# Kernel optimization log

Measured on AMD Instinct MI355X. Metric: run time of the kernel, lower is better.

## Reference

```python
import jax, jax.numpy as jnp
import numpy as np

WIN = 8        # window_size
HEADS = 8      # n_heads
SHIFT = WIN // 2

# relative position index (static buffer, n_dim=2)
_coords = np.stack(np.meshgrid(np.arange(WIN), np.arange(WIN), indexing='ij'), 0).reshape(2, WIN * WIN)
_rel = _coords[:, :, None] - _coords[:, None, :] + (WIN - 1)          # [2, w*w, w*w]
REL_IDX = _rel[0] * (2 * WIN - 1) + _rel[1]                            # [w*w, w*w] int


def setup_inputs() -> dict:
    key = jax.random.key(0)
    ks = jax.random.split(key, 6)
    B, C, H, W = 4, 256, 128, 128
    x = jax.random.normal(ks[0], (B, C, H, W), dtype=jnp.float32)
    w_qkv = jax.random.normal(ks[1], (C, 3 * C), dtype=jnp.float32) * 0.02
    b_qkv = jax.random.normal(ks[2], (3 * C,), dtype=jnp.float32) * 0.02
    w_out = jax.random.normal(ks[3], (C, C), dtype=jnp.float32) * 0.02
    b_out = jax.random.normal(ks[4], (C,), dtype=jnp.float32) * 0.02
    bias_table = jax.random.normal(ks[5], ((2 * WIN - 1) ** 2, HEADS), dtype=jnp.float32) * 0.02
    return {"x": x, "w_qkv": w_qkv, "b_qkv": b_qkv, "w_out": w_out, "b_out": b_out, "bias_table": bias_table}


def reference(x, w_qkv, b_qkv, w_out, b_out, bias_table):
    B, C, H, W = x.shape
    w = WIN
    ch = C // HEADS
    xf = jnp.moveaxis(x, 1, -1)                                # [B,H,W,C]
    xf = jnp.roll(xf, (-SHIFT, -SHIFT), axis=(1, 2))           # shifted windows (cyclic)
    # H,W chosen divisible by window_size -> no circular padding needed
    qkv = xf @ w_qkv + b_qkv                                   # [B,H,W,3C]
    Hw, Ww = H // w, W // w
    # contiguous window partition -> [B, nWin, w*w, 3, heads, ch]
    qkv = qkv.reshape(B, Hw, w, Ww, w, 3 * C).transpose(0, 1, 3, 2, 4, 5)
    qkv = qkv.reshape(B, Hw * Ww, w * w, 3, HEADS, ch)
    q = jnp.moveaxis(qkv[..., 0, :, :], -2, 2)                 # [B,nWin,heads,seq,ch]
    k = jnp.moveaxis(qkv[..., 1, :, :], -2, 2)
    v = jnp.moveaxis(qkv[..., 2, :, :], -2, 2)
    bias = bias_table[REL_IDX]                                 # [seq,seq,heads]
    bias = jnp.transpose(bias, (2, 0, 1))                      # [heads,seq,seq]
    scale = 1.0 / jnp.sqrt(jnp.asarray(ch, dtype=q.dtype))
    scores = jnp.einsum('bnhsc,bnhtc->bnhst', q, k) * scale + bias
    attn = jax.nn.softmax(scores, axis=-1)
    out = jnp.einsum('bnhst,bnhtc->bnhsc', attn, v)            # [B,nWin,heads,seq,ch]
    out = jnp.moveaxis(out, 2, -2).reshape(B, Hw, Ww, w, w, C) # merge heads
    out = out.transpose(0, 1, 3, 2, 4, 5).reshape(B, H, W, C)  # un-window
    out = jnp.roll(out, (SHIFT, SHIFT), axis=(1, 2))           # undo shift
    out = out @ w_out + b_out                                  # [B,H,W,Cout]
    return jnp.moveaxis(out, -1, 1)                            # [B,Cout,H,W]
```

## Files before the change

### kernel.cpp

```cpp
#include <hip/hip_runtime.h>

typedef float  f32x4  __attribute__((ext_vector_type(4)));
typedef __bf16 bf16x8 __attribute__((ext_vector_type(8)));
typedef __bf16 bf16x2 __attribute__((ext_vector_type(2)));
typedef short  s16x8  __attribute__((ext_vector_type(8)));
typedef unsigned u32x4 __attribute__((ext_vector_type(4)));

static __device__ __forceinline__ unsigned short f2bf(float f) {
  unsigned u = __builtin_bit_cast(unsigned, f);
  u += 0x7FFFu + ((u >> 16) & 1u);
  return (unsigned short)(u >> 16);
}

static __device__ __forceinline__ unsigned pk2(float a, float b) {
  bf16x2 v = { (__bf16)a, (__bf16)b };
  return __builtin_bit_cast(unsigned, v);
}

static __device__ __forceinline__ f32x4 mfma16(s16x8 a, s16x8 b, f32x4 c) {
  return __builtin_amdgcn_mfma_f32_16x16x32_bf16(
      __builtin_bit_cast(bf16x8, a), __builtin_bit_cast(bf16x8, b), c, 0, 0, 0);
}

static __device__ __forceinline__ void gll16(const void* g, void* lds) {
  __builtin_amdgcn_global_load_lds(
      (const __attribute__((address_space(1))) unsigned int*)g,
      (__attribute__((address_space(3))) unsigned int*)lds, 16, 0, 0);
}

__global__ __launch_bounds__(256) void k_conv_x(const float* __restrict__ x,
                                                unsigned short* __restrict__ xb) {
  __shared__ __align__(16) unsigned short L[512 * 40];
  int bid = blockIdx.x;
  int cchunk = bid & 7, h2 = (bid >> 3) & 1, wy = (bid >> 4) & 15, b = bid >> 8;
  int t = threadIdx.x;
  int cpair = t >> 7, slot = t & 127, lr = slot >> 5, lp = slot & 31;
  int y = (wy * 8 + h2 * 4 + lr + 4) & 127;
  const float* row0 = x + ((size_t)b << 22) + (y << 7);
  int cbase = cchunk * 32;

  for (int it = 0; it < 8; ++it) {
    int cL0 = it * 4 + cpair * 2;
    const float* pa = row0 + ((size_t)(cbase + cL0) << 14) + lp * 4;
    f32x4 a  = *reinterpret_cast<const f32x4*>(pa);
    f32x4 c4 = *reinterpret_cast<const f32x4*>(pa + 16384);
#pragma unroll
    for (int i = 0; i < 4; ++i) {
      int xc = lp * 4 + i;
      int xp = (xc - 4) & 127;
      int wx = xp >> 3, ix = xp & 7;
      int sg = lr * 128 + ix * 16 + wx;
      unsigned pk = (unsigned)f2bf(a[i]) | ((unsigned)f2bf(c4[i]) << 16);
      *reinterpret_cast<unsigned*>(&L[sg * 40 + cL0]) = pk;
    }
  }
  __syncthreads();

  size_t M0 = ((size_t)((b * 16 + wy) * 16)) * 64 + h2 * 32;
  for (int pass = 0; pass < 8; ++pass) {
    int tk = pass * 64 + (t >> 2), p = t & 3;
    int wx = tk >> 5, lr2 = (tk >> 3) & 3, ix = tk & 7;
    int sg = lr2 * 128 + ix * 16 + wx;
    uint4 v = *reinterpret_cast<const uint4*>(&L[sg * 40 + p * 8]);
    size_t m = M0 + (size_t)wx * 64 + lr2 * 8 + ix;
    *reinterpret_cast<uint4*>(&xb[m * 256 + cbase + p * 8]) = v;
  }
}

__global__ __launch_bounds__(256) void k_conv_w(const float* __restrict__ wqkv,
                                                const float* __restrict__ wout,
                                                unsigned short* __restrict__ wqkvT,
                                                unsigned short* __restrict__ woutT) {
  int j = blockIdx.x, c = threadIdx.x;
  if (j < 768) wqkvT[j * 256 + c] = f2bf(wqkv[c * 768 + j]);
  else { int jj = j - 768; woutT[jj * 256 + c] = f2bf(wout[c * 256 + jj]); }
}

__global__ __launch_bounds__(256) void k_bias(const float* __restrict__ btab,
                                              float* __restrict__ bmat) {
  int i = blockIdx.x * 256 + threadIdx.x;
  int t = i & 63, s = (i >> 6) & 63, h = i >> 12;
  int idx = ((s >> 3) - (t >> 3) + 7) * 15 + ((s & 7) - (t & 7) + 7);
  bmat[i] = btab[idx * 8 + h];
}

__global__ __launch_bounds__(256, 4) void k_qkvattn(const unsigned short* __restrict__ xb,
                                                    const unsigned short* __restrict__ wT,
                                                    const float* __restrict__ bqkv,
                                                    const float* __restrict__ bmat,
                                                    unsigned short* __restrict__ ao) {
  __shared__ __align__(16) unsigned char smA[32768];
  int lane = threadIdx.x & 63, w = threadIdx.x >> 6;
  int bid = blockIdx.x;
  int sb = (bid & 7) * 256 + (bid >> 3);
  int win = sb >> 1, h = (sb & 1) * 4 + w;
  int g = lane >> 4, l15 = lane & 15;
  int m0 = win * 64;
  const float scale = 0.17677669529663687f;

#pragma unroll
  for (int i = 0; i < 8; ++i) {
    int inst = w * 8 + i;
    int row = inst * 2 + (lane >> 5);
    int sg = (lane & 31) ^ (row & 7);
    gll16(xb + (size_t)(m0 + row) * 256 + sg * 8, smA + inst * 1024);
  }
  __syncthreads();

  const unsigned short* Wq = wT + (size_t)(h * 32 + l15) * 256 + g * 8;
  const unsigned short* Wk = Wq + 65536;
  const unsigned short* Wv = Wk + 65536;

  f32x4 aQ[2][4], aK[2][4];
#pragma unroll
  for (int jt = 0; jt < 2; ++jt)
#pragma unroll
    for (int mt = 0; mt < 4; ++mt) {
      aQ[jt][mt] = f32x4{0.f, 0.f, 0.f, 0.f};
      aK[jt][mt] = f32x4{0.f, 0.f, 0.f, 0.f};
    }
#pragma unroll
  for (int ks = 0; ks < 8; ++ks) {
    int off = ks * 32;
    s16x8 fq[2], fk[2];
#pragma unroll
    for (int jt = 0; jt < 2; ++jt) {
      fq[jt] = *reinterpret_cast<const s16x8*>(Wq + (size_t)jt * 4096 + off);
      fk[jt] = *reinterpret_cast<const s16x8*>(Wk + (size_t)jt * 4096 + off);
    }
    s16x8 af[4];
#pragma unroll
    for (int mt = 0; mt < 4; ++mt) {
      int row = mt * 16 + l15;
      int chunk = (ks * 4 + g) ^ (row & 7);
      af[mt] = *reinterpret_cast<const s16x8*>(smA + row * 512 + chunk * 16);
    }
    __builtin_amdgcn_s_setprio(1);
#pragma unroll
    for (int jt = 0; jt < 2; ++jt)
#pragma unroll
      for (int mt = 0; mt < 4; ++mt) {
        aQ[jt][mt] = mfma16(fq[jt], af[mt], aQ[jt][mt]);
        aK[jt][mt] = mfma16(fk[jt], af[mt], aK[jt][mt]);
      }
    __builtin_amdgcn_s_setprio(0);
  }

  f32x4 bq2[2], bk2[2];
#pragma unroll
  for (int jt = 0; jt < 2; ++jt) {
    bq2[jt] = *reinterpret_cast<const f32x4*>(&bqkv[h * 32 + jt * 16 + g * 4]);
    bk2[jt] = *reinterpret_cast<const f32x4*>(&bqkv[256 + h * 32 + jt * 16 + g * 4]);
  }
  s16x8 kfr[4], qfr[4];
#pragma unroll
  for (int ti = 0; ti < 4; ++ti) {
    u32x4 uk, uq;
    uk[0] = pk2(aK[0][ti][0] + bk2[0][0], aK[0][ti][1] + bk2[0][1]);
    uk[1] = pk2(aK[0][ti][2] + bk2[0][2], aK[0][ti][3] + bk2[0][3]);
    uk[2] = pk2(aK[1][ti][0] + bk2[1][0], aK[1][ti][1] + bk2[1][1]);
    uk[3] = pk2(aK[1][ti][2] + bk2[1][2], aK[1][ti][3] + bk2[1][3]);
    kfr[ti] = __builtin_bit_cast(s16x8, uk);
    uq[0] = pk2((aQ[0][ti][0] + bq2[0][0]) * scale, (aQ[0][ti][1] + bq2[0][1]) * scale);
    uq[1] = pk2((aQ[0][ti][2] + bq2[0][2]) * scale, (aQ[0][ti][3] + bq2[0][3]) * scale);
    uq[2] = pk2((aQ[1][ti][0] + bq2[1][0]) * scale, (aQ[1][ti][1] + bq2[1][1]) * scale);
    uq[3] = pk2((aQ[1][ti][2] + bq2[1][2]) * scale, (aQ[1][ti][3] + bq2[1][3]) * scale);
    qfr[ti] = __builtin_bit_cast(s16x8, uq);
  }

  f32x4 aV[4][2];
#pragma unroll
  for (int mt = 0; mt < 4; ++mt)
#pragma unroll
    for (int ni = 0; ni < 2; ++ni) aV[mt][ni] = f32x4{0.f, 0.f, 0.f, 0.f};
#pragma unroll
  for (int ks = 0; ks < 8; ++ks) {
    int off = ks * 32;
    s16x8 fv[2];
#pragma unroll
    for (int jt = 0; jt < 2; ++jt)
      fv[jt] = *reinterpret_cast<const s16x8*>(Wv + (size_t)jt * 4096 + off);
    s16x8 af[4];
#pragma unroll
    for (int mt = 0; mt < 4; ++mt) {
      int row = mt * 16 + l15;
      int chunk = (ks * 4 + g) ^ (row & 7);
      af[mt] = *reinterpret_cast<const s16x8*>(smA + row * 512 + chunk * 16);
    }
    __builtin_amdgcn_s_setprio(1);
#pragma unroll
    for (int mt = 0; mt < 4; ++mt)
#pragma unroll
      for (int ni = 0; ni < 2; ++ni)
        aV[mt][ni] = mfma16(af[mt], fv[ni], aV[mt][ni]);
    __builtin_amdgcn_s_setprio(0);
  }

  float bv2[2];
  bv2[0] = bqkv[512 + h * 32 + l15];
  bv2[1] = bqkv[512 + h * 32 + 16 + l15];
  s16x8 vfr[2][2];
#pragma unroll
  for (int ni = 0; ni < 2; ++ni)
#pragma unroll
    for (int ks = 0; ks < 2; ++ks) {
      u32x4 uv;
      uv[0] = pk2(aV[2 * ks][ni][0] + bv2[ni], aV[2 * ks][ni][1] + bv2[ni]);
      uv[1] = pk2(aV[2 * ks][ni][2] + bv2[ni], aV[2 * ks][ni][3] + bv2[ni]);
      uv[2] = pk2(aV[2 * ks + 1][ni][0] + bv2[ni], aV[2 * ks + 1][ni][1] + bv2[ni]);
      uv[3] = pk2(aV[2 * ks + 1][ni][2] + bv2[ni], aV[2 * ks + 1][ni][3] + bv2[ni]);
      vfr[ni][ks] = __builtin_bit_cast(s16x8, uv);
    }

  const float* bm = bmat + (h << 12);
  f32x4 sbf[4][4];
#pragma unroll
  for (int ti = 0; ti < 4; ++ti)
#pragma unroll
    for (int si = 0; si < 4; ++si)
      sbf[ti][si] = *reinterpret_cast<const f32x4*>(&bm[(si * 16 + l15) * 64 + ti * 16 + g * 4]);

  f32x4 st[4][4];
  __builtin_amdgcn_s_setprio(1);
#pragma unroll
  for (int ti = 0; ti < 4; ++ti)
#pragma unroll
    for (int si = 0; si < 4; ++si)
      st[ti][si] = mfma16(kfr[ti], qfr[si], sbf[ti][si]);
  __builtin_amdgcn_s_setprio(0);

  unsigned pw[4][4][2];
#pragma unroll
  for (int si = 0; si < 4; ++si) {
    float mx = st[0][si][0];
#pragma unroll
    for (int ti = 0; ti < 4; ++ti)
#pragma unroll
      for (int r = 0; r < 4; ++r) mx = fmaxf(mx, st[ti][si][r]);
    mx = fmaxf(mx, __shfl_xor(mx, 16));
    mx = fmaxf(mx, __shfl_xor(mx, 32));
    float p[4][4];
    float sum = 0.f;
#pragma unroll
    for (int ti = 0; ti < 4; ++ti)
#pragma unroll
      for (int r = 0; r < 4; ++r) {
        p[ti][r] = __expf(st[ti][si][r] - mx);
        sum += p[ti][r];
      }
    sum += __shfl_xor(sum, 16);
    sum += __shfl_xor(sum, 32);
    float inv = 1.0f / sum;
#pragma unroll
    for (int ti = 0; ti < 4; ++ti) {
      pw[ti][si][0] = pk2(p[ti][0] * inv, p[ti][1] * inv);
      pw[ti][si][1] = pk2(p[ti][2] * inv, p[ti][3] * inv);
    }
  }

  f32x4 ot[2][4];
#pragma unroll
  for (int ni = 0; ni < 2; ++ni)
#pragma unroll
    for (int mi = 0; mi < 4; ++mi) ot[ni][mi] = f32x4{0.f, 0.f, 0.f, 0.f};
  __builtin_amdgcn_s_setprio(1);
#pragma unroll
  for (int ks = 0; ks < 2; ++ks) {
#pragma unroll
    for (int mi = 0; mi < 4; ++mi) {
      u32x4 up;
      up[0] = pw[2 * ks][mi][0];
      up[1] = pw[2 * ks][mi][1];
      up[2] = pw[2 * ks + 1][mi][0];
      up[3] = pw[2 * ks + 1][mi][1];
      s16x8 pf = __builtin_bit_cast(s16x8, up);
#pragma unroll
      for (int ni = 0; ni < 2; ++ni)
        ot[ni][mi] = mfma16(vfr[ni][ks], pf, ot[ni][mi]);
    }
  }
  __builtin_amdgcn_s_setprio(0);

#pragma unroll
  for (int ni = 0; ni < 2; ++ni)
#pragma unroll
    for (int mi = 0; mi < 4; ++mi) {
      uint2 pk;
      pk.x = pk2(ot[ni][mi][0], ot[ni][mi][1]);
      pk.y = pk2(ot[ni][mi][2], ot[ni][mi][3]);
      size_t m = (size_t)(win * 64 + mi * 16 + l15);
      *reinterpret_cast<uint2*>(&ao[m * 256 + h * 32 + ni * 16 + g * 4]) = pk;
    }
}

__global__ __launch_bounds__(256) void k_oproj(const unsigned short* __restrict__ ao,
                                               const unsigned short* __restrict__ wT,
                                               const float* __restrict__ bout,
                                               float* __restrict__ out) {
  __shared__ __align__(16) unsigned short Al[128 * 64];
  __shared__ __align__(16) unsigned short Bl[128 * 64];
  int j0 = blockIdx.x * 128, m0 = blockIdx.y * 128;
  int lane = threadIdx.x & 63, w = threadIdx.x >> 6;
  int wm = w >> 1, wn = w & 1, g = lane >> 4, l15 = lane & 15;

  f32x4 acc[4][4];
#pragma unroll
  for (int i = 0; i < 4; ++i)
#pragma unroll
    for (int j = 0; j < 4; ++j) acc[i][j] = f32x4{0.f, 0.f, 0.f, 0.f};

  for (int kt = 0; kt < 4; ++kt) {
    int k0 = kt * 64;
#pragma unroll
    for (int i = 0; i < 4; ++i) {
      int r0 = (w * 4 + i) * 8;
      int row = r0 + (lane >> 3);
      int sg = (lane & 7) ^ (row & 7);
      gll16(ao + (size_t)(m0 + row) * 256 + k0 + sg * 8, &Al[r0 * 64]);
      gll16(wT + (size_t)(j0 + row) * 256 + k0 + sg * 8, &Bl[r0 * 64]);
    }
    __syncthreads();
#pragma unroll
    for (int ks = 0; ks < 2; ++ks) {
      s16x8 af[4], bf[4];
#pragma unroll
      for (int mi = 0; mi < 4; ++mi) {
        int row = wm * 64 + mi * 16 + l15;
        int chunk = (ks * 4 + g) ^ (row & 7);
        af[mi] = *reinterpret_cast<const s16x8*>(&Al[row * 64 + chunk * 8]);
      }
#pragma unroll
      for (int ni = 0; ni < 4; ++ni) {
        int row = wn * 64 + ni * 16 + l15;
        int chunk = (ks * 4 + g) ^ (row & 7);
        bf[ni] = *reinterpret_cast<const s16x8*>(&Bl[row * 64 + chunk * 8]);
      }
#pragma unroll
      for (int mi = 0; mi < 4; ++mi)
#pragma unroll
        for (int ni = 0; ni < 4; ++ni)
          acc[mi][ni] = mfma16(af[mi], bf[ni], acc[mi][ni]);
    }
    __syncthreads();
  }

#pragma unroll
  for (int ni = 0; ni < 4; ++ni) {
    int j = j0 + wn * 64 + ni * 16 + l15;
    float bj = bout[j];
#pragma unroll
    for (int mi = 0; mi < 4; ++mi) {
      int mb = m0 + wm * 64 + mi * 16 + g * 4;
      int win = mb >> 6, seq0 = mb & 63;
      int b = win >> 8, wy = (win >> 4) & 15, wx = win & 15;
      int iy = seq0 >> 3, ix0 = seq0 & 7;
      int y = (wy * 8 + iy + 4) & 127;
      int x0 = (wx * 8 + ix0 + 4) & 127;
      f32x4 v = acc[mi][ni];
      v.x += bj; v.y += bj; v.z += bj; v.w += bj;
      *reinterpret_cast<f32x4*>(&out[(((size_t)b * 256 + j) << 14) + (y << 7) + x0]) = v;
    }
  }
}

extern "C" void kernel_launch(void* const* d_in, const int* in_sizes, int n_in,
                              void* d_out, int out_size, void* d_ws, size_t ws_size,
                              hipStream_t stream) {
  const float* x    = (const float*)d_in[0];
  const float* wqkv = (const float*)d_in[1];
  const float* bqkv = (const float*)d_in[2];
  const float* wout = (const float*)d_in[3];
  const float* bout = (const float*)d_in[4];
  const float* btab = (const float*)d_in[5];
  float* out = (float*)d_out;
  char* ws = (char*)d_ws;

  unsigned short* XB = (unsigned short*)(ws);
  unsigned short* AO = (unsigned short*)(ws + 33554432);
  unsigned short* WQ = (unsigned short*)(ws + 67108864);
  unsigned short* WO = (unsigned short*)(ws + 67502080);
  float*          BM = (float*)(ws + 67633152);
  if (ws_size < 67764224ull) return;

  k_conv_x<<<1024, 256, 0, stream>>>(x, XB);
  k_conv_w<<<1024, 256, 0, stream>>>(wqkv, wout, WQ, WO);
  k_bias<<<128, 256, 0, stream>>>(btab, BM);
  k_qkvattn<<<2048, 256, 0, stream>>>(XB, WQ, bqkv, BM, AO);
  k_oproj<<<dim3(2, 512), 256, 0, stream>>>(AO, WO, bout, out);
}
```

Before: 137.6 us.

## Split window attention into two key halves with online softmax rescaling

The 64-key score computation is split into two 32-key halves. Each half computes scores, does a partial softmax and immediately feeds its P·V MFMA, and the second half rescales the running output and sum in the flash-attention style. Normalization by the final sum moves to the output store. This lowers register pressure, since only a half score tile and not the full 4x4 tile plus bias is live at once, and it lets MFMA overlap with softmax ALU work. The cost is extra exp and rescale operations and more shuffles.

Measured after the change: 135.0 us. Within noise of the previous version (-1.9%).

```diff
diff --git a/kernel.cpp b/kernel.cpp
--- a/kernel.cpp
+++ b/kernel.cpp
@@ -213,81 +213,98 @@
     }
 
   const float* bm = bmat + (h << 12);
-  f32x4 sbf[4][4];
-#pragma unroll
-  for (int ti = 0; ti < 4; ++ti)
-#pragma unroll
-    for (int si = 0; si < 4; ++si)
-      sbf[ti][si] = *reinterpret_cast<const f32x4*>(&bm[(si * 16 + l15) * 64 + ti * 16 + g * 4]);
-
-  f32x4 st[4][4];
-  __builtin_amdgcn_s_setprio(1);
-#pragma unroll
-  for (int ti = 0; ti < 4; ++ti)
-#pragma unroll
-    for (int si = 0; si < 4; ++si)
-      st[ti][si] = mfma16(kfr[ti], qfr[si], sbf[ti][si]);
-  __builtin_amdgcn_s_setprio(0);
-
-  unsigned pw[4][4][2];
-#pragma unroll
-  for (int si = 0; si < 4; ++si) {
-    float mx = st[0][si][0];
-#pragma unroll
-    for (int ti = 0; ti < 4; ++ti)
-#pragma unroll
-      for (int r = 0; r < 4; ++r) mx = fmaxf(mx, st[ti][si][r]);
-    mx = fmaxf(mx, __shfl_xor(mx, 16));
-    mx = fmaxf(mx, __shfl_xor(mx, 32));
-    float p[4][4];
-    float sum = 0.f;
-#pragma unroll
-    for (int ti = 0; ti < 4; ++ti)
-#pragma unroll
-      for (int r = 0; r < 4; ++r) {
-        p[ti][r] = __expf(st[ti][si][r] - mx);
-        sum += p[ti][r];
-      }
-    sum += __shfl_xor(sum, 16);
-    sum += __shfl_xor(sum, 32);
-    float inv = 1.0f / sum;
-#pragma unroll
-    for (int ti = 0; ti < 4; ++ti) {
-      pw[ti][si][0] = pk2(p[ti][0] * inv, p[ti][1] * inv);
-      pw[ti][si][1] = pk2(p[ti][2] * inv, p[ti][3] * inv);
-    }
-  }
-
   f32x4 ot[2][4];
 #pragma unroll
   for (int ni = 0; ni < 2; ++ni)
 #pragma unroll
     for (int mi = 0; mi < 4; ++mi) ot[ni][mi] = f32x4{0.f, 0.f, 0.f, 0.f};
-  __builtin_amdgcn_s_setprio(1);
-#pragma unroll
-  for (int ks = 0; ks < 2; ++ks) {
+
+  float m01[4], s01[4], inv[4];
+
+  {
+    f32x4 sth[2][4];
+    __builtin_amdgcn_s_setprio(1);
+#pragma unroll
+    for (int th = 0; th < 2; ++th)
+#pragma unroll
+      for (int si = 0; si < 4; ++si)
+        sth[th][si] = mfma16(kfr[th], qfr[si], f32x4{0.f, 0.f, 0.f, 0.f});
+    __builtin_amdgcn_s_setprio(0);
+#pragma unroll
+    for (int si = 0; si < 4; ++si) {
+      int srow = (si * 16 + l15) * 64;
+      f32x4 v0 = sth[0][si] + *reinterpret_cast<const f32x4*>(&bm[srow + g * 4]);
+      f32x4 v1 = sth[1][si] + *reinterpret_cast<const f32x4*>(&bm[srow + 16 + g * 4]);
+      float mx = fmaxf(fmaxf(fmaxf(v0[0], v0[1]), fmaxf(v0[2], v0[3])),
+                       fmaxf(fmaxf(v1[0], v1[1]), fmaxf(v1[2], v1[3])));
+      mx = fmaxf(mx, __shfl_xor(mx, 16));
+      mx = fmaxf(mx, __shfl_xor(mx, 32));
+      f32x4 p0, p1;
+      float sum = 0.f;
+#pragma unroll
+      for (int r = 0; r < 4; ++r) { p0[r] = __expf(v0[r] - mx); sum += p0[r]; }
+#pragma unroll
+      for (int r = 0; r < 4; ++r) { p1[r] = __expf(v1[r] - mx); sum += p1[r]; }
+      sum += __shfl_xor(sum, 16);
+      sum += __shfl_xor(sum, 32);
+      m01[si] = mx; s01[si] = sum;
+      u32x4 up;
+      up[0] = pk2(p0[0], p0[1]); up[1] = pk2(p0[2], p0[3]);
+      up[2] = pk2(p1[0], p1[1]); up[3] = pk2(p1[2], p1[3]);
+      s16x8 pf = __builtin_bit_cast(s16x8, up);
+      ot[0][si] = mfma16(vfr[0][0], pf, ot[0][si]);
+      ot[1][si] = mfma16(vfr[1][0], pf, ot[1][si]);
+    }
+  }
+
+  {
+    f32x4 sth[2][4];
+    __builtin_amdgcn_s_setprio(1);
+#pragma unroll
+    for (int th = 0; th < 2; ++th)
+#pragma unroll
+      for (int si = 0; si < 4; ++si)
+        sth[th][si] = mfma16(kfr[2 + th], qfr[si], f32x4{0.f, 0.f, 0.f, 0.f});
+    __builtin_amdgcn_s_setprio(0);
+#pragma unroll
+    for (int si = 0; si < 4; ++si) {
+      int srow = (si * 16 + l15) * 64;
+      f32x4 v0 = sth[0][si] + *reinterpret_cast<const f32x4*>(&bm[srow + 32 + g * 4]);
+      f32x4 v1 = sth[1][si] + *reinterpret_cast<const f32x4*>(&bm[srow + 48 + g * 4]);
+      float m23 = fmaxf(fmaxf(fmaxf(v0[0], v0[1]), fmaxf(v0[2], v0[3])),
+                        fmaxf(fmaxf(v1[0], v1[1]), fmaxf(v1[2], v1[3])));
+      m23 = fmaxf(m23, __shfl_xor(m23, 16));
+      m23 = fmaxf(m23, __shfl_xor(m23, 32));
+      float m = fmaxf(m01[si], m23);
+      float c01 = __expf(m01[si] - m);
+      f32x4 p0, p1;
+      float sum = 0.f;
+#pragma unroll
+      for (int r = 0; r < 4; ++r) { p0[r] = __expf(v0[r] - m); sum += p0[r]; }
+#pragma unroll
+      for (int r = 0; r < 4; ++r) { p1[r] = __expf(v1[r] - m); sum += p1[r]; }
+      sum += __shfl_xor(sum, 16);
+      sum += __shfl_xor(sum, 32);
+      inv[si] = 1.0f / (c01 * s01[si] + sum);
+      u32x4 up;
+      up[0] = pk2(p0[0], p0[1]); up[1] = pk2(p0[2], p0[3]);
+      up[2] = pk2(p1[0], p1[1]); up[3] = pk2(p1[2], p1[3]);
+      s16x8 pf = __builtin_bit_cast(s16x8, up);
+      ot[0][si] *= c01;
+      ot[1][si] *= c01;
+      ot[0][si] = mfma16(vfr[0][1], pf, ot[0][si]);
+      ot[1][si] = mfma16(vfr[1][1], pf, ot[1][si]);
+    }
+  }
+
+#pragma unroll
+  for (int ni = 0; ni < 2; ++ni)
 #pragma unroll
     for (int mi = 0; mi < 4; ++mi) {
-      u32x4 up;
-      up[0] = pw[2 * ks][mi][0];
-      up[1] = pw[2 * ks][mi][1];
-      up[2] = pw[2 * ks + 1][mi][0];
-      up[3] = pw[2 * ks + 1][mi][1];
-      s16x8 pf = __builtin_bit_cast(s16x8, up);
-#pragma unroll
-      for (int ni = 0; ni < 2; ++ni)
-        ot[ni][mi] = mfma16(vfr[ni][ks], pf, ot[ni][mi]);
-    }
-  }
-  __builtin_amdgcn_s_setprio(0);
-
-#pragma unroll
-  for (int ni = 0; ni < 2; ++ni)
-#pragma unroll
-    for (int mi = 0; mi < 4; ++mi) {
+      float iv = inv[mi];
       uint2 pk;
-      pk.x = pk2(ot[ni][mi][0], ot[ni][mi][1]);
-      pk.y = pk2(ot[ni][mi][2], ot[ni][mi][3]);
+      pk.x = pk2(ot[ni][mi][0] * iv, ot[ni][mi][1] * iv);
+      pk.y = pk2(ot[ni][mi][2] * iv, ot[ni][mi][3] * iv);
       size_t m = (size_t)(win * 64 + mi * 16 + l15);
       *reinterpret_cast<uint2*>(&ao[m * 256 + h * 32 + ni * 16 + g * 4]) = pk;
     }
```
